# Optimization experiments

Measured on AMD Instinct MI355X. Metric: run time of the kernel, lower is better.

The kernel has to match this reference:

```python
import jax, jax.numpy as jnp
import numpy as np

HIDDEN = 1024

def setup_inputs() -> dict:
    key = jax.random.key(0)
    ks = jax.random.split(key, 7)
    B, S, H = 4, 4096, HIDDEN
    scale = 1.0 / np.sqrt(H)
    return {
        "x": jax.random.normal(ks[0], (B, S, H), dtype=jnp.float32),
        "Wq": jax.random.normal(ks[1], (H, H), dtype=jnp.float32) * scale,
        "bq": jnp.zeros((H,), dtype=jnp.float32),
        "Wk": jax.random.normal(ks[2], (H, H), dtype=jnp.float32) * scale,
        "bk": jnp.zeros((H,), dtype=jnp.float32),
        "Wv": jax.random.normal(ks[3], (H, H), dtype=jnp.float32) * scale,
        "bv": jnp.zeros((H,), dtype=jnp.float32),
    }

def reference(x, Wq, bq, Wk, bk, Wv, bv):
    # Linear layers: y = x @ W^T + b (torch nn.Linear convention)
    q = jnp.einsum('bsh,oh->bso', x, Wq) + bq
    k = jnp.einsum('bsh,oh->bso', x, Wk) + bk
    v = jnp.einsum('bsh,oh->bso', x, Wv) + bv
    # NOTE: source applies NO 1/sqrt(d) scaling — faithful reproduction.
    scores = jnp.einsum('bqh,bkh->bqk', q, k)  # [B,S,S]
    attn = jax.nn.softmax(scores, axis=-1)
    return jnp.einsum('bqk,bkh->bqh', attn, v)
```

## Files before the change

### kernel.cpp

```cpp
#include <hip/hip_runtime.h>
#include <math.h>
#include <type_traits>


typedef unsigned short u16;
typedef _Float16 f16x8 __attribute__((ext_vector_type(8)));
typedef __bf16 bf16x8 __attribute__((ext_vector_type(8)));
typedef float f32x4 __attribute__((ext_vector_type(4)));
struct __align__(8) u16x4 { u16 x, y, z, w; };

__device__ __forceinline__ u16 f2bf(float f) {
    unsigned u = __builtin_bit_cast(unsigned, f);
    u += 0x7fffu + ((u >> 16) & 1u);
    return (u16)(u >> 16);
}
__device__ __forceinline__ u16 f2h(float f) {
    _Float16 h = (_Float16)f;
    return __builtin_bit_cast(u16, h);
}
__device__ __forceinline__ float h2f(u16 h) {
    return (float)__builtin_bit_cast(_Float16, h);
}

#define MF16(a, b, c) __builtin_amdgcn_mfma_f32_16x16x32_f16( \
    __builtin_bit_cast(f16x8, a), __builtin_bit_cast(f16x8, b), c, 0, 0, 0)
#define MBF16(a, b, c) __builtin_amdgcn_mfma_f32_16x16x32_bf16(a, b, c, 0, 0, 0)

#define SLOT_E  (4u * 1024 * 1024)
#define BBLK_E  (16u * 1024 * 1024)

__global__ __launch_bounds__(512, 4) void gemm_projqk(
    const u16* __restrict__ xh, const u16* __restrict__ xl,
    const u16* __restrict__ Wq, const u16* __restrict__ Wk,
    const float* __restrict__ bq, const float* __restrict__ bk,
    u16* __restrict__ qout, u16* __restrict__ kout)
{
    __shared__ char lds[4 * 8192];
    const int K = 1024, lda = 1024, ldb = 1024, ldc = 1024, nbx = 8;

    const int cpx = (int)gridDim.x >> 3;
    const int raw = blockIdx.x;
    const int swz = (raw & 7) * cpx + (raw >> 3);
    const int bm = (swz / nbx) * 128, bn = (swz % nbx) * 128;

    const int t = threadIdx.x;
    const int w = t >> 6, lane = t & 63;
    const int qksel = w >> 2;
    const int wl = w & 3;
    const int wr = wl >> 1, wc = wl & 1;
    const int r16 = lane & 15, g = lane >> 4;

    f32x4 acc[4][4];
#pragma unroll
    for (int i = 0; i < 4; ++i)
#pragma unroll
        for (int j = 0; j < 4; ++j) acc[i][j] = (f32x4)0.0f;

    for (int k0 = 0; k0 < K; k0 += 32) {
#pragma unroll
        for (int i = 0; i < 4; ++i) {
            const int ch = w * 4 + i;
            const int tt = ch >> 3, sub = ch & 7;
            const int s = sub * 64 + lane;
            const int row = s >> 2;
            const int kg = (s & 3) ^ ((row >> 1) & 3);
            const u16* P = (tt == 0) ? xh : (tt == 1) ? xl : (tt == 2) ? Wq : Wk;
            const int rbase = (tt < 2) ? bm : bn;
            const int ld = (tt < 2) ? lda : ldb;
            __builtin_amdgcn_global_load_lds(
                (const __attribute__((address_space(1))) void*)
                    (P + (size_t)(rbase + row) * ld + k0 + kg * 8),
                (__attribute__((address_space(3))) void*)(lds + ch * 1024),
                16, 0, 0);
        }
        __syncthreads();

        bf16x8 fa[2][4], fb[4];
#pragma unroll
        for (int i = 0; i < 4; ++i) {
            const int ra = wr * 64 + i * 16 + r16;
            const int oa = ra * 64 + ((g ^ ((ra >> 1) & 3)) << 4);
            fa[0][i] = *(const bf16x8*)(lds + oa);
            fa[1][i] = *(const bf16x8*)(lds + 8192 + oa);
            const int rbw = wc * 64 + i * 16 + r16;
            const int ob = rbw * 64 + ((g ^ ((rbw >> 1) & 3)) << 4);
            fb[i] = *(const bf16x8*)(lds + (2 + qksel) * 8192 + ob);
        }
#pragma unroll
        for (int i = 0; i < 4; ++i)
#pragma unroll
            for (int j = 0; j < 4; ++j) {
                acc[i][j] = MF16(fa[0][i], fb[j], acc[i][j]);
                acc[i][j] = MF16(fa[1][i], fb[j], acc[i][j]);
            }
        __syncthreads();
    }

    u16* Cout = qksel ? kout : qout;
    const float* bias = qksel ? bk : bq;
#pragma unroll
    for (int j = 0; j < 4; ++j) {
        const int gc = bn + wc * 64 + j * 16 + r16;
        const float bv = bias[gc];
#pragma unroll
        for (int i = 0; i < 4; ++i) {
            const int gr = bm + wr * 64 + i * 16 + g * 4;
#pragma unroll
            for (int r = 0; r < 4; ++r) {
                const int grr = gr + r;
                const size_t bb = (size_t)(grr >> 12) * BBLK_E;
                Cout[bb + (size_t)(grr & 4095) * ldc + gc] = f2h(acc[i][j][r] + bv);
            }
        }
    }
}

#define GEMM_PARAMS const u16* __restrict__ A0, const u16* __restrict__ A1, \
    const u16* __restrict__ B0, \
    int K, int lda, int ldb, const float* __restrict__ bias, \
    float* __restrict__ Cf, u16* __restrict__ Ch, \
    int ldc, int nbx, unsigned long long zsA, unsigned long long zsB, \
    unsigned long long zsC

template<int VAR, int DEPTH>
__device__ __forceinline__ void gemm_pipe_body(GEMM_PARAMS)
{
    __shared__ char lds[(DEPTH + 1) * 16384];

    const int cpx = (int)gridDim.x >> 3;
    const int raw = blockIdx.x;
    const int swz = (raw & 7) * cpx + (raw >> 3);
    const int bm = (swz / nbx) * 128, bn = (swz % nbx) * 128;

    const unsigned long long z = blockIdx.z;
    A0 += z * zsA;
    B0 += z * zsB;

    const int t = threadIdx.x;
    const int w = t >> 6, lane = t & 63;
    const int wr = w >> 1, wc = w & 1;
    const int r16 = lane & 15, g = lane >> 4;

    f32x4 acc[4][4];
#pragma unroll
    for (int i = 0; i < 4; ++i)
#pragma unroll
        for (int j = 0; j < 4; ++j) acc[i][j] = (f32x4)0.0f;

    auto STAGE = [&](auto BO, int k0) {
#pragma unroll
        for (int i = 0; i < 4; ++i) {
            constexpr int bufo = decltype(BO)::value;
            const int ch = w * 4 + i;
            const int tt = ch >> 3, sub = ch & 7;
            const int s = sub * 64 + lane;
            const int row = s >> 2;
            const int kg = (s & 3) ^ ((row >> 1) & 3);
            const u16* P = tt ? B0 : A0;
            const int rbase = tt ? bn : bm;
            const int ld = tt ? ldb : lda;
            __builtin_amdgcn_global_load_lds(
                (const __attribute__((address_space(1))) void*)
                    (P + (size_t)(rbase + row) * ld + k0 + kg * 8),
                (__attribute__((address_space(3))) void*)(lds + bufo + ch * 1024),
                16, 0, 0);
        }
    };

    bf16x8 fa[4], fb[4];
    auto FRAGS = [&](auto BO) {
        constexpr int bufo = decltype(BO)::value;
#pragma unroll
        for (int i = 0; i < 4; ++i) {
            const int ra = wr * 64 + i * 16 + r16;
            fa[i] = *(const bf16x8*)(lds + bufo + ra * 64 + ((g ^ ((ra >> 1) & 3)) << 4));
            const int rbw = wc * 64 + i * 16 + r16;
            fb[i] = *(const bf16x8*)(lds + bufo + 8192 + rbw * 64 + ((g ^ ((rbw >> 1) & 3)) << 4));
        }
    };
    auto MM = [&]() {
#pragma unroll
        for (int i = 0; i < 4; ++i)
#pragma unroll
            for (int j = 0; j < 4; ++j) {
                if constexpr (VAR == 3) acc[i][j] = MBF16(fa[i], fb[j], acc[i][j]);
                else                    acc[i][j] = MF16(fa[i], fb[j], acc[i][j]);
            }
    };

    std::integral_constant<int, 0> c0;
    std::integral_constant<int, 16384> c1;
    std::integral_constant<int, 32768> c2;

    const int nk = K >> 5;

    if constexpr (DEPTH == 1) {
        STAGE(c0, 0);
        STAGE(c1, 1 << 5);
        for (int tt = 0; tt + 2 < nk; tt += 2) {
            asm volatile("s_waitcnt vmcnt(4)\n\ts_barrier" ::: "memory");
            FRAGS(c0);
            asm volatile("s_waitcnt lgkmcnt(0)\n\ts_barrier" ::: "memory");
            STAGE(c0, (tt + 2) << 5);
            MM();
            asm volatile("s_waitcnt vmcnt(4)\n\ts_barrier" ::: "memory");
            FRAGS(c1);
            asm volatile("s_waitcnt lgkmcnt(0)\n\ts_barrier" ::: "memory");
            STAGE(c1, (tt + 3) << 5);
            MM();
        }
        asm volatile("s_waitcnt vmcnt(4)\n\ts_barrier" ::: "memory");
        FRAGS(c0);
        MM();
        asm volatile("s_waitcnt vmcnt(0)\n\ts_barrier" ::: "memory");
        FRAGS(c1);
        MM();
    } else {
        STAGE(c0, 0);
        STAGE(c1, 1 << 5);
        STAGE(c2, 2 << 5);
        for (int tt = 0; tt + 4 < nk; tt += 3) {
            asm volatile("s_waitcnt vmcnt(8)\n\ts_barrier" ::: "memory");
            FRAGS(c0);
            asm volatile("s_waitcnt lgkmcnt(0)\n\ts_barrier" ::: "memory");
            STAGE(c0, (tt + 3) << 5);
            MM();
            asm volatile("s_waitcnt vmcnt(8)\n\ts_barrier" ::: "memory");
            FRAGS(c1);
            asm volatile("s_waitcnt lgkmcnt(0)\n\ts_barrier" ::: "memory");
            STAGE(c1, (tt + 4) << 5);
            MM();
            asm volatile("s_waitcnt vmcnt(8)\n\ts_barrier" ::: "memory");
            FRAGS(c2);
            asm volatile("s_waitcnt lgkmcnt(0)\n\ts_barrier" ::: "memory");
            if (tt + 5 < nk) STAGE(c2, (tt + 5) << 5);
            MM();
        }
        asm volatile("s_waitcnt vmcnt(4)\n\ts_barrier" ::: "memory");
        FRAGS(c0);
        MM();
        asm volatile("s_waitcnt vmcnt(0)\n\ts_barrier" ::: "memory");
        FRAGS(c1);
        MM();
    }

#pragma unroll
    for (int j = 0; j < 4; ++j) {
        const int gc = bn + wc * 64 + j * 16 + r16;
        const float bv = bias ? bias[gc] : 0.0f;
#pragma unroll
        for (int i = 0; i < 4; ++i) {
            const int gr = bm + wr * 64 + i * 16 + g * 4;
#pragma unroll
            for (int r = 0; r < 4; ++r) {
                const float val = acc[i][j][r] + bv;
                const int grr = gr + r;
                if constexpr (VAR == 1) {
                    Ch[(size_t)gc * ldc + grr] = f2bf(val);
                } else {
                    Cf[z * zsC + (size_t)grr * ldc + gc] = val;
                }
            }
        }
    }
}

__global__ __launch_bounds__(256) void gemm_projv(GEMM_PARAMS) { gemm_pipe_body<1, 1>(A0,A1,B0,K,lda,ldb,bias,Cf,Ch,ldc,nbx,zsA,zsB,zsC); }
__global__ __launch_bounds__(256) void gemm_scores(GEMM_PARAMS){ gemm_pipe_body<2, 1>(A0,A1,B0,K,lda,ldb,bias,Cf,Ch,ldc,nbx,zsA,zsB,zsC); }
__global__ __launch_bounds__(256) void gemm_pv(GEMM_PARAMS)    { gemm_pipe_body<3, 2>(A0,A1,B0,K,lda,ldb,bias,Cf,Ch,ldc,nbx,zsA,zsB,zsC); }

__global__ __launch_bounds__(256) void split_h(
    const float* __restrict__ in, u16* __restrict__ hi, u16* __restrict__ lo, int n4)
{
    const int i = blockIdx.x * 256 + threadIdx.x;
    if (i >= n4) return;
    const float4 v = ((const float4*)in)[i];
    u16x4 h, l;
    h.x = f2h(v.x); l.x = f2h(v.x - h2f(h.x));
    h.y = f2h(v.y); l.y = f2h(v.y - h2f(h.y));
    h.z = f2h(v.z); l.z = f2h(v.z - h2f(h.z));
    h.w = f2h(v.w); l.w = f2h(v.w - h2f(h.w));
    ((u16x4*)hi)[i] = h;
    ((u16x4*)lo)[i] = l;
}

__global__ __launch_bounds__(256) void softmax4096(
    const float* __restrict__ S, u16* __restrict__ P)
{
    const float* p = S + (size_t)blockIdx.x * 4096;
    u16* q = P + (size_t)blockIdx.x * 4096;
    const int t = threadIdx.x;
    const int wave = t >> 6, lane = t & 63;
    __shared__ float red[8];

    float4 v[4];
    float mx = -INFINITY;
#pragma unroll
    for (int i = 0; i < 4; ++i) {
        v[i] = ((const float4*)p)[i * 256 + t];
        mx = fmaxf(mx, fmaxf(fmaxf(v[i].x, v[i].y), fmaxf(v[i].z, v[i].w)));
    }
#pragma unroll
    for (int o = 32; o > 0; o >>= 1) mx = fmaxf(mx, __shfl_xor(mx, o));
    if (lane == 0) red[wave] = mx;
    __syncthreads();
    mx = fmaxf(fmaxf(red[0], red[1]), fmaxf(red[2], red[3]));

    float sum = 0.f;
#pragma unroll
    for (int i = 0; i < 4; ++i) {
        v[i].x = __expf(v[i].x - mx);
        v[i].y = __expf(v[i].y - mx);
        v[i].z = __expf(v[i].z - mx);
        v[i].w = __expf(v[i].w - mx);
        sum += (v[i].x + v[i].y) + (v[i].z + v[i].w);
    }
#pragma unroll
    for (int o = 32; o > 0; o >>= 1) sum += __shfl_xor(sum, o);
    if (lane == 0) red[4 + wave] = sum;
    __syncthreads();
    sum = (red[4] + red[5]) + (red[6] + red[7]);

    const float inv = 1.0f / sum;
#pragma unroll
    for (int i = 0; i < 4; ++i) {
        u16x4 u;
        u.x = f2bf(v[i].x * inv); u.y = f2bf(v[i].y * inv);
        u.z = f2bf(v[i].z * inv); u.w = f2bf(v[i].w * inv);
        ((u16x4*)q)[i * 256 + t] = u;
    }
}

extern "C" void kernel_launch(void* const* d_in, const int* in_sizes, int n_in,
                              void* d_out, int out_size, void* d_ws, size_t ws_size,
                              hipStream_t stream)
{
    const float* x  = (const float*)d_in[0];
    const float* Wq = (const float*)d_in[1];
    const float* bq = (const float*)d_in[2];
    const float* Wk = (const float*)d_in[3];
    const float* bk = (const float*)d_in[4];
    const float* Wv = (const float*)d_in[5];
    const float* bv = (const float*)d_in[6];
    float* out = (float*)d_out;

    const int B = 4, S = 4096, H = 1024;
    const size_t MB = 1u << 20;
    if (ws_size < 256 * MB) return;
    char* wsp = (char*)d_ws;

    u16* xh = (u16*)(wsp);
    u16* xl = (u16*)(wsp + 32 * MB);
    float* sc = (float*)(wsp);
    u16* qk = (u16*)(wsp + 64 * MB);
    u16* vT = (u16*)(wsp + 192 * MB);
    u16* Wqh = (u16*)(wsp + 224 * MB), *Wql = (u16*)(wsp + 226 * MB);
    u16* Wkh = (u16*)(wsp + 228 * MB), *Wkl = (u16*)(wsp + 230 * MB);
    u16* Wvh = (u16*)(wsp + 232 * MB), *Wvl = (u16*)(wsp + 234 * MB);

    const dim3 blk(256);
    const u16* nul16 = nullptr;
    float* nulf = nullptr;

    hipLaunchKernelGGL(split_h, dim3(B * S * H / 4 / 256), blk, 0, stream, x, xh, xl, B * S * H / 4);
    hipLaunchKernelGGL(split_h, dim3(H * H / 4 / 256), blk, 0, stream, Wq, Wqh, Wql, H * H / 4);
    hipLaunchKernelGGL(split_h, dim3(H * H / 4 / 256), blk, 0, stream, Wk, Wkh, Wkl, H * H / 4);
    hipLaunchKernelGGL(split_h, dim3(H * H / 4 / 256), blk, 0, stream, Wv, Wvh, Wvl, H * H / 4);

    hipLaunchKernelGGL(gemm_projqk, dim3(1024), dim3(512), 0, stream,
        xh, xl, Wqh, Wkh, bq, bk,
        qk + 0 * SLOT_E, qk + 1 * SLOT_E);
    hipLaunchKernelGGL(gemm_projv, dim3(1024), blk, 0, stream,
        xh, nul16, Wvh, H, H, H, bv,
        nulf, vT, B * S, 8, 0ull, 0ull, 0ull);

    for (int b = 0; b < B; ++b) {
        const u16* qb = qk + (size_t)b * BBLK_E;
        hipLaunchKernelGGL(gemm_scores, dim3(1024), blk, 0, stream,
            qb, nul16, qb + SLOT_E,
            H, H, H, (const float*)nullptr,
            sc, (u16*)nullptr, S, 32, 0ull, 0ull, 0ull);
        hipLaunchKernelGGL(softmax4096, dim3(S), blk, 0, stream,
            sc, qk + (size_t)b * BBLK_E);
    }

    hipLaunchKernelGGL(gemm_pv, dim3(256, 1, 4), blk, 0, stream,
        qk, nul16, vT,
        S, S, B * S, (const float*)nullptr,
        out, (u16*)nullptr, H, 8,
        (unsigned long long)BBLK_E, 4096ull, (unsigned long long)S * H);
}
```

Measured before the change: 637.0 us.

## Use 512-thread 128x256 tiles for projection, scores and PV GEMMs

The shared GEMM body moves from 256-thread blocks computing 128x128 tiles to 512-thread blocks (8 waves in a 2x4 layout) computing 128x256 tiles. Each k-step now stages 24 KB into LDS with a simple double buffer, and the 3-stage pipeline the PV GEMM used is dropped. Grids are halved to match. The aim is more reuse of the A tile and fewer blocks. In exchange it uses more LDS per block, has a shallower pipeline for PV, and gives fewer blocks per GEMM, which may hurt load balance.

```diff
diff --git a/kernel.cpp b/kernel.cpp
--- a/kernel.cpp
+++ b/kernel.cpp
@@ -115,22 +115,21 @@
     }
 }
 
-#define GEMM_PARAMS const u16* __restrict__ A0, const u16* __restrict__ A1, \
-    const u16* __restrict__ B0, \
+#define GEMM_PARAMS const u16* __restrict__ A0, const u16* __restrict__ B0, \
     int K, int lda, int ldb, const float* __restrict__ bias, \
     float* __restrict__ Cf, u16* __restrict__ Ch, \
     int ldc, int nbx, unsigned long long zsA, unsigned long long zsB, \
     unsigned long long zsC
 
-template<int VAR, int DEPTH>
-__device__ __forceinline__ void gemm_pipe_body(GEMM_PARAMS)
-{
-    __shared__ char lds[(DEPTH + 1) * 16384];
+template<int VAR>
+__device__ __forceinline__ void gemm8_body(GEMM_PARAMS)
+{
+    __shared__ char lds[2 * 24576];
 
     const int cpx = (int)gridDim.x >> 3;
     const int raw = blockIdx.x;
     const int swz = (raw & 7) * cpx + (raw >> 3);
-    const int bm = (swz / nbx) * 128, bn = (swz % nbx) * 128;
+    const int bm = (swz / nbx) * 128, bn = (swz % nbx) * 256;
 
     const unsigned long long z = blockIdx.z;
     A0 += z * zsA;
@@ -138,7 +137,7 @@
 
     const int t = threadIdx.x;
     const int w = t >> 6, lane = t & 63;
-    const int wr = w >> 1, wc = w & 1;
+    const int wr = w >> 2, wc = w & 3;
     const int r16 = lane & 15, g = lane >> 4;
 
     f32x4 acc[4][4];
@@ -149,20 +148,21 @@
 
     auto STAGE = [&](auto BO, int k0) {
 #pragma unroll
-        for (int i = 0; i < 4; ++i) {
+        for (int i = 0; i < 3; ++i) {
             constexpr int bufo = decltype(BO)::value;
-            const int ch = w * 4 + i;
-            const int tt = ch >> 3, sub = ch & 7;
-            const int s = sub * 64 + lane;
-            const int row = s >> 2;
-            const int kg = (s & 3) ^ ((row >> 1) & 3);
-            const u16* P = tt ? B0 : A0;
-            const int rbase = tt ? bn : bm;
-            const int ld = tt ? ldb : lda;
+            const int ch = w * 3 + i;
+            const int isB = (ch >= 8);
+            const int cb = isB ? (ch - 8) : ch;
+            const int row = cb * 16 + (lane >> 2);
+            const int kg = (lane & 3) ^ ((row >> 1) & 3);
+            const u16* P = isB ? B0 : A0;
+            const int rbase = isB ? bn : bm;
+            const int ld = isB ? ldb : lda;
             __builtin_amdgcn_global_load_lds(
                 (const __attribute__((address_space(1))) void*)
                     (P + (size_t)(rbase + row) * ld + k0 + kg * 8),
-                (__attribute__((address_space(3))) void*)(lds + bufo + ch * 1024),
+                (__attribute__((address_space(3))) void*)
+                    (lds + bufo + (isB ? 8192 : 0) + cb * 1024),
                 16, 0, 0);
         }
     };
@@ -174,8 +174,8 @@
         for (int i = 0; i < 4; ++i) {
             const int ra = wr * 64 + i * 16 + r16;
             fa[i] = *(const bf16x8*)(lds + bufo + ra * 64 + ((g ^ ((ra >> 1) & 3)) << 4));
-            const int rbw = wc * 64 + i * 16 + r16;
-            fb[i] = *(const bf16x8*)(lds + bufo + 8192 + rbw * 64 + ((g ^ ((rbw >> 1) & 3)) << 4));
+            const int rb = wc * 64 + i * 16 + r16;
+            fb[i] = *(const bf16x8*)(lds + bufo + 8192 + rb * 64 + ((g ^ ((rb >> 1) & 3)) << 4));
         }
     };
     auto MM = [&]() {
@@ -189,60 +189,29 @@
     };
 
     std::integral_constant<int, 0> c0;
-    std::integral_constant<int, 16384> c1;
-    std::integral_constant<int, 32768> c2;
+    std::integral_constant<int, 24576> c1;
 
     const int nk = K >> 5;
-
-    if constexpr (DEPTH == 1) {
-        STAGE(c0, 0);
-        STAGE(c1, 1 << 5);
-        for (int tt = 0; tt + 2 < nk; tt += 2) {
-            asm volatile("s_waitcnt vmcnt(4)\n\ts_barrier" ::: "memory");
-            FRAGS(c0);
-            asm volatile("s_waitcnt lgkmcnt(0)\n\ts_barrier" ::: "memory");
-            STAGE(c0, (tt + 2) << 5);
-            MM();
-            asm volatile("s_waitcnt vmcnt(4)\n\ts_barrier" ::: "memory");
-            FRAGS(c1);
-            asm volatile("s_waitcnt lgkmcnt(0)\n\ts_barrier" ::: "memory");
-            STAGE(c1, (tt + 3) << 5);
-            MM();
-        }
-        asm volatile("s_waitcnt vmcnt(4)\n\ts_barrier" ::: "memory");
+    STAGE(c0, 0);
+    STAGE(c1, 1 << 5);
+    for (int tt = 0; tt + 2 < nk; tt += 2) {
+        asm volatile("s_waitcnt vmcnt(3)\n\ts_barrier" ::: "memory");
         FRAGS(c0);
+        asm volatile("s_waitcnt lgkmcnt(0)\n\ts_barrier" ::: "memory");
+        STAGE(c0, (tt + 2) << 5);
         MM();
-        asm volatile("s_waitcnt vmcnt(0)\n\ts_barrier" ::: "memory");
+        asm volatile("s_waitcnt vmcnt(3)\n\ts_barrier" ::: "memory");
         FRAGS(c1);
+        asm volatile("s_waitcnt lgkmcnt(0)\n\ts_barrier" ::: "memory");
+        STAGE(c1, (tt + 3) << 5);
         MM();
-    } else {
-        STAGE(c0, 0);
-        STAGE(c1, 1 << 5);
-        STAGE(c2, 2 << 5);
-        for (int tt = 0; tt + 4 < nk; tt += 3) {
-            asm volatile("s_waitcnt vmcnt(8)\n\ts_barrier" ::: "memory");
-            FRAGS(c0);
-            asm volatile("s_waitcnt lgkmcnt(0)\n\ts_barrier" ::: "memory");
-            STAGE(c0, (tt + 3) << 5);
-            MM();
-            asm volatile("s_waitcnt vmcnt(8)\n\ts_barrier" ::: "memory");
-            FRAGS(c1);
-            asm volatile("s_waitcnt lgkmcnt(0)\n\ts_barrier" ::: "memory");
-            STAGE(c1, (tt + 4) << 5);
-            MM();
-            asm volatile("s_waitcnt vmcnt(8)\n\ts_barrier" ::: "memory");
-            FRAGS(c2);
-            asm volatile("s_waitcnt lgkmcnt(0)\n\ts_barrier" ::: "memory");
-            if (tt + 5 < nk) STAGE(c2, (tt + 5) << 5);
-            MM();
-        }
-        asm volatile("s_waitcnt vmcnt(4)\n\ts_barrier" ::: "memory");
-        FRAGS(c0);
-        MM();
-        asm volatile("s_waitcnt vmcnt(0)\n\ts_barrier" ::: "memory");
-        FRAGS(c1);
-        MM();
-    }
+    }
+    asm volatile("s_waitcnt vmcnt(3)\n\ts_barrier" ::: "memory");
+    FRAGS(c0);
+    MM();
+    asm volatile("s_waitcnt vmcnt(0)\n\ts_barrier" ::: "memory");
+    FRAGS(c1);
+    MM();
 
 #pragma unroll
     for (int j = 0; j < 4; ++j) {
@@ -265,9 +234,9 @@
     }
 }
 
-__global__ __launch_bounds__(256) void gemm_projv(GEMM_PARAMS) { gemm_pipe_body<1, 1>(A0,A1,B0,K,lda,ldb,bias,Cf,Ch,ldc,nbx,zsA,zsB,zsC); }
-__global__ __launch_bounds__(256) void gemm_scores(GEMM_PARAMS){ gemm_pipe_body<2, 1>(A0,A1,B0,K,lda,ldb,bias,Cf,Ch,ldc,nbx,zsA,zsB,zsC); }
-__global__ __launch_bounds__(256) void gemm_pv(GEMM_PARAMS)    { gemm_pipe_body<3, 2>(A0,A1,B0,K,lda,ldb,bias,Cf,Ch,ldc,nbx,zsA,zsB,zsC); }
+__global__ __launch_bounds__(512, 4) void gemm_projv(GEMM_PARAMS) { gemm8_body<1>(A0,B0,K,lda,ldb,bias,Cf,Ch,ldc,nbx,zsA,zsB,zsC); }
+__global__ __launch_bounds__(512, 4) void gemm_scores(GEMM_PARAMS){ gemm8_body<2>(A0,B0,K,lda,ldb,bias,Cf,Ch,ldc,nbx,zsA,zsB,zsC); }
+__global__ __launch_bounds__(512, 4) void gemm_pv(GEMM_PARAMS)    { gemm8_body<3>(A0,B0,K,lda,ldb,bias,Cf,Ch,ldc,nbx,zsA,zsB,zsC); }
 
 __global__ __launch_bounds__(256) void split_h(
     const float* __restrict__ in, u16* __restrict__ hi, u16* __restrict__ lo, int n4)
@@ -359,7 +328,6 @@
     u16* Wvh = (u16*)(wsp + 232 * MB), *Wvl = (u16*)(wsp + 234 * MB);
 
     const dim3 blk(256);
-    const u16* nul16 = nullptr;
     float* nulf = nullptr;
 
     hipLaunchKernelGGL(split_h, dim3(B * S * H / 4 / 256), blk, 0, stream, x, xh, xl, B * S * H / 4);
@@ -370,23 +338,23 @@
     hipLaunchKernelGGL(gemm_projqk, dim3(1024), dim3(512), 0, stream,
         xh, xl, Wqh, Wkh, bq, bk,
         qk + 0 * SLOT_E, qk + 1 * SLOT_E);
-    hipLaunchKernelGGL(gemm_projv, dim3(1024), blk, 0, stream,
-        xh, nul16, Wvh, H, H, H, bv,
-        nulf, vT, B * S, 8, 0ull, 0ull, 0ull);
+    hipLaunchKernelGGL(gemm_projv, dim3(512), dim3(512), 0, stream,
+        xh, Wvh, H, H, H, bv,
+        nulf, vT, B * S, 4, 0ull, 0ull, 0ull);
 
     for (int b = 0; b < B; ++b) {
         const u16* qb = qk + (size_t)b * BBLK_E;
-        hipLaunchKernelGGL(gemm_scores, dim3(1024), blk, 0, stream,
-            qb, nul16, qb + SLOT_E,
+        hipLaunchKernelGGL(gemm_scores, dim3(512), dim3(512), 0, stream,
+            qb, qb + SLOT_E,
             H, H, H, (const float*)nullptr,
-            sc, (u16*)nullptr, S, 32, 0ull, 0ull, 0ull);
+            sc, (u16*)nullptr, S, 16, 0ull, 0ull, 0ull);
         hipLaunchKernelGGL(softmax4096, dim3(S), blk, 0, stream,
             sc, qk + (size_t)b * BBLK_E);
     }
 
-    hipLaunchKernelGGL(gemm_pv, dim3(256, 1, 4), blk, 0, stream,
-        qk, nul16, vT,
+    hipLaunchKernelGGL(gemm_pv, dim3(128, 1, 4), dim3(512), 0, stream,
+        qk, vT,
         S, S, B * S, (const float*)nullptr,
-        out, (u16*)nullptr, H, 8,
+        out, (u16*)nullptr, H, 4,
         (unsigned long long)BBLK_E, 4096ull, (unsigned long long)S * H);
 }
```

After: 563.1 us, median of 5. 1.13x faster.
